# Kernel optimization log

Measured on AMD Instinct MI355X. Metric: run time of the kernel, lower is better.

Reference implementation:

```python
import jax, jax.numpy as jnp
from jax import lax
import numpy as np

B, T, S = 64, 1024, 1024  # batch, seq_len, hidden size


def setup_inputs() -> dict:
    key = jax.random.key(0)
    ks = jax.random.split(key, 7)
    bound = 1.0 / np.sqrt(S)  # PyTorch GRU/Linear default init: U(-1/sqrt(H), 1/sqrt(H))
    u = lambda k, shape: jax.random.uniform(k, shape, jnp.float32, -bound, bound)
    return {
        "batch": jax.random.normal(ks[0], (B, T, S), jnp.float32),
        "W_ih": u(ks[1], (3 * S, S)),   # [r; z; n] input weights
        "W_hh": u(ks[2], (3 * S, S)),   # [r; z; n] hidden weights
        "b_ih": u(ks[3], (3 * S,)),
        "b_hh": u(ks[4], (3 * S,)),
        "W_out": u(ks[5], (1, S)),
        "b_out": u(ks[6], (1,)),
    }


def reference(batch, W_ih, W_hh, b_ih, b_hh, W_out, b_out):
    # Precompute input projections for all timesteps with one big GEMM: [B,T,3S]
    x_gates = jnp.einsum("bts,gs->btg", batch, W_ih) + b_ih

    def step(h, xg):
        # h: [B,S], xg: [B,3S]
        hg = h @ W_hh.T + b_hh                      # [B,3S]
        xr, xz, xn = jnp.split(xg, 3, axis=-1)
        hr, hz, hn = jnp.split(hg, 3, axis=-1)
        r = jax.nn.sigmoid(xr + hr)
        z = jax.nn.sigmoid(xz + hz)
        n = jnp.tanh(xn + r * hn)
        h_new = (1.0 - z) * n + z * h               # PyTorch GRU update
        return h_new, None

    h0 = jnp.zeros((batch.shape[0], S), batch.dtype)
    hT, _ = lax.scan(step, h0, jnp.swapaxes(x_gates, 0, 1))  # scan over time

    # last-timestep hidden -> linear -> sigmoid -> squeeze
    out = jax.nn.sigmoid(hT @ W_out.T + b_out)  # [B,1]
    return out.squeeze(-1)                      # [B]
```

## Files before the change

kernel.cpp:

```cpp
#include <hip/hip_runtime.h>
#include <math.h>


#define BB 64
#define TT 1024
#define SS 1024
#define GG (3 * SS)
#define NBLK 256

__device__ unsigned g_sub[8 * 32];
__device__ unsigned g_cnt[32];
__device__ unsigned g_gen[32];

__global__ void init_bar_kernel() {
  for (int i = 0; i < 8 * 32; ++i) g_sub[i] = 0u;
  g_cnt[0] = 0u;
  g_gen[0] = 0u;
}

__global__ void zero_kernel(float* __restrict__ p) {
  p[(size_t)blockIdx.x * 1024 + threadIdx.x] = 0.f;
}

__global__ __launch_bounds__(256) void xgates_kernel(
    const float* __restrict__ A, const float* __restrict__ W,
    const float* __restrict__ b_ih, const float* __restrict__ b_hh,
    float* __restrict__ C) {
  __shared__ float As[16][132];
  __shared__ float Bs[16][132];

  const int tid = threadIdx.x;
  const int n0 = blockIdx.x * 128;
  const int t0 = blockIdx.y * 2;
  const int tx = tid & 15;
  const int ty = tid >> 4;

  float acc[8][8];
#pragma unroll
  for (int i = 0; i < 8; ++i)
#pragma unroll
    for (int j = 0; j < 8; ++j) acc[i][j] = 0.f;

  for (int kt = 0; kt < SS / 16; ++kt) {
    const int k0 = kt * 16;
#pragma unroll
    for (int i = 0; i < 2; ++i) {
      const int idx = tid + i * 256;
      const int r = idx >> 2;
      const int kq = (idx & 3) * 4;
      float4 av = *(const float4*)&A[((size_t)(r & 63) * TT + t0 + (r >> 6)) * SS + k0 + kq];
      float4 bv = *(const float4*)&W[(size_t)(n0 + r) * SS + k0 + kq];
      As[kq + 0][r] = av.x; As[kq + 1][r] = av.y;
      As[kq + 2][r] = av.z; As[kq + 3][r] = av.w;
      Bs[kq + 0][r] = bv.x; Bs[kq + 1][r] = bv.y;
      Bs[kq + 2][r] = bv.z; Bs[kq + 3][r] = bv.w;
    }
    __syncthreads();
#pragma unroll
    for (int k = 0; k < 16; ++k) {
      float4 a0 = *(const float4*)&As[k][ty * 8];
      float4 a1 = *(const float4*)&As[k][ty * 8 + 4];
      float4 b0 = *(const float4*)&Bs[k][tx * 8];
      float4 b1 = *(const float4*)&Bs[k][tx * 8 + 4];
      float a[8] = {a0.x, a0.y, a0.z, a0.w, a1.x, a1.y, a1.z, a1.w};
      float b[8] = {b0.x, b0.y, b0.z, b0.w, b1.x, b1.y, b1.z, b1.w};
#pragma unroll
      for (int i = 0; i < 8; ++i)
#pragma unroll
        for (int j = 0; j < 8; ++j) acc[i][j] = fmaf(a[i], b[j], acc[i][j]);
    }
    __syncthreads();
  }

  float bias[8];
#pragma unroll
  for (int j = 0; j < 8; ++j) {
    const int n = n0 + tx * 8 + j;
    bias[j] = b_ih[n] + (n < 2 * SS ? b_hh[n] : 0.f);
  }
  const int tt = t0 + (ty >> 3);
  const int bbase = (ty & 7) * 8;
#pragma unroll
  for (int j = 0; j < 8; ++j) {
    const int n = n0 + tx * 8 + j;
    const int g = n >> 10;
    const int u = n & 1023;
    const size_t o = ((size_t)(tt * 3 + g) * SS + u) * 64 + bbase;
    *(float4*)&C[o] = make_float4(acc[0][j] + bias[j], acc[1][j] + bias[j],
                                  acc[2][j] + bias[j], acc[3][j] + bias[j]);
    *(float4*)&C[o + 4] = make_float4(acc[4][j] + bias[j], acc[5][j] + bias[j],
                                      acc[6][j] + bias[j], acc[7][j] + bias[j]);
  }
}

__global__ __launch_bounds__(1024) void gru_persistent(
    const float* __restrict__ Whh, const float* __restrict__ xgT,
    const float* __restrict__ bhh, float* hA, float* hB) {
  __shared__ float part[16][64][13];
  __shared__ float sums[64][13];

  const int tid = threadIdx.x;
  const int lane = tid & 63;
  const int u0 = blockIdx.x * 4;
  const int wv = __builtin_amdgcn_readfirstlane(tid >> 6);
  const int k0 = wv * 64;
  const int ur = tid >> 6;

  const float* Wrow[12];
#pragma unroll
  for (int g = 0; g < 3; ++g)
#pragma unroll
    for (int r = 0; r < 4; ++r)
      Wrow[g * 4 + r] = Whh + (size_t)(g * SS + u0 + r) * SS + k0;

  float bhn = 0.f, xr = 0.f, xz = 0.f, xn = 0.f;
  if (tid < 256) {
    bhn = bhh[2 * SS + u0 + ur];
    const size_t xb = (size_t)(u0 + ur) * 64 + (size_t)lane;
    xr = xgT[xb];
    xz = xgT[xb + (size_t)SS * 64];
    xn = xgT[xb + (size_t)2 * SS * 64];
  }

  for (int t = 0; t < TT; ++t) {
    float* hin = (t & 1) ? hB : hA;
    float* hout = (t & 1) ? hA : hB;

    float hold = 0.f;
    if (tid < 256)
      hold = __hip_atomic_load(&hin[(u0 + ur) * 64 + lane], __ATOMIC_RELAXED,
                               __HIP_MEMORY_SCOPE_AGENT);

    float acc[12];
#pragma unroll
    for (int i = 0; i < 12; ++i) acc[i] = 0.f;

    for (int kk = 0; kk < 64; kk += 8) {
      float hv[8];
#pragma unroll
      for (int e = 0; e < 8; ++e)
        hv[e] = __hip_atomic_load(&hin[(size_t)(k0 + kk + e) * 64 + lane],
                                  __ATOMIC_RELAXED, __HIP_MEMORY_SCOPE_AGENT);
#pragma unroll
      for (int i = 0; i < 12; ++i) {
        const float* wp = Wrow[i] + kk;
        const float4 wa = *(const float4*)wp;
        const float4 wb = *(const float4*)(wp + 4);
        float a = acc[i];
        a = fmaf(hv[0], wa.x, a);
        a = fmaf(hv[1], wa.y, a);
        a = fmaf(hv[2], wa.z, a);
        a = fmaf(hv[3], wa.w, a);
        a = fmaf(hv[4], wb.x, a);
        a = fmaf(hv[5], wb.y, a);
        a = fmaf(hv[6], wb.z, a);
        a = fmaf(hv[7], wb.w, a);
        acc[i] = a;
      }
    }

    const int w = tid >> 6;
#pragma unroll
    for (int i = 0; i < 12; ++i) part[w][lane][i] = acc[i];
    __syncthreads();

    if (tid < 768) {
      const int sb = tid & 63, si = tid >> 6;
      float v = 0.f;
#pragma unroll
      for (int ww = 0; ww < 16; ++ww) v += part[ww][sb][si];
      sums[sb][si] = v;
    }
    __syncthreads();

    if (tid < 256) {
      const float ar = sums[lane][ur];
      const float az = sums[lane][4 + ur];
      const float an = sums[lane][8 + ur];
      const float rg = 1.f / (1.f + expf(-(xr + ar)));
      const float zg = 1.f / (1.f + expf(-(xz + az)));
      const float ng = tanhf(xn + rg * (an + bhn));
      const float hnew = (1.f - zg) * ng + zg * hold;
      __hip_atomic_store(&hout[(u0 + ur) * 64 + lane], hnew, __ATOMIC_RELAXED,
                         __HIP_MEMORY_SCOPE_AGENT);
      if (t + 1 < TT) {
        const size_t xb =
            ((size_t)((t + 1) * 3) * SS + u0 + ur) * 64 + (size_t)lane;
        xr = xgT[xb];
        xz = xgT[xb + (size_t)SS * 64];
        xn = xgT[xb + (size_t)2 * SS * 64];
      }
    }

    if (t != TT - 1) {
      __syncthreads();
      if (tid == 0) {
        bool done = false;
        const unsigned a = atomicAdd(&g_sub[(blockIdx.x & 7) * 32], 1u);
        if (a == 32u * (unsigned)(t + 1) - 1u) {
          const unsigned g = atomicAdd(&g_cnt[0], 1u);
          if (g == 8u * (unsigned)(t + 1) - 1u) {
            __hip_atomic_store(&g_gen[0], (unsigned)(t + 1), __ATOMIC_RELAXED,
                               __HIP_MEMORY_SCOPE_AGENT);
            done = true;
          }
        }
        if (!done) {
          while (__hip_atomic_load(&g_gen[0], __ATOMIC_RELAXED,
                                   __HIP_MEMORY_SCOPE_AGENT) <
                 (unsigned)(t + 1))
            __builtin_amdgcn_s_sleep(2);
        }
        __builtin_amdgcn_fence(__ATOMIC_ACQUIRE, "workgroup");
      }
      __syncthreads();
    }
  }
}

__global__ __launch_bounds__(256) void out_kernel(
    const float* __restrict__ hT, const float* __restrict__ Wout,
    const float* __restrict__ bout, float* __restrict__ out) {
  const int b = blockIdx.x;
  const int tid = threadIdx.x;
  float s = 0.f;
#pragma unroll
  for (int i = 0; i < 4; ++i) {
    const int u = tid + i * 256;
    s = fmaf(hT[(size_t)u * 64 + b], Wout[u], s);
  }
#pragma unroll
  for (int off = 32; off; off >>= 1) s += __shfl_down(s, off);
  __shared__ float red[4];
  if ((tid & 63) == 0) red[tid >> 6] = s;
  __syncthreads();
  if (tid == 0) {
    const float tot = red[0] + red[1] + red[2] + red[3] + bout[0];
    out[b] = 1.f / (1.f + expf(-tot));
  }
}

extern "C" void kernel_launch(void* const* d_in, const int* in_sizes, int n_in,
                              void* d_out, int out_size, void* d_ws,
                              size_t ws_size, hipStream_t stream) {
  const float* batch = (const float*)d_in[0];
  const float* W_ih = (const float*)d_in[1];
  const float* W_hh = (const float*)d_in[2];
  const float* b_ih = (const float*)d_in[3];
  const float* b_hh = (const float*)d_in[4];
  const float* W_out = (const float*)d_in[5];
  const float* b_out = (const float*)d_in[6];
  float* out = (float*)d_out;

  float* xgT = (float*)d_ws;
  float* hA = xgT + (size_t)TT * GG * BB;
  float* hB = hA + (size_t)SS * BB;

  init_bar_kernel<<<1, 1, 0, stream>>>();
  zero_kernel<<<BB, 1024, 0, stream>>>(hA);

  xgates_kernel<<<dim3(GG / 128, (BB * TT) / 128), 256, 0, stream>>>(
      batch, W_ih, b_ih, b_hh, xgT);

  {
    const float* a0 = W_hh;
    const float* a1 = xgT;
    const float* a2 = b_hh;
    float* a3 = hA;
    float* a4 = hB;
    void* args[5] = {&a0, &a1, &a2, &a3, &a4};
    hipLaunchCooperativeKernel((const void*)gru_persistent, dim3(NBLK),
                               dim3(1024), args, 0, stream);
  }

  out_kernel<<<BB, 256, 0, stream>>>(hA, W_out, b_out, out);
}
```

Before: 17.20 ms.

## Interleave hidden state layout for 64-bit loads, keep h in registers, prefetch x-gates

Changes the hidden-state buffer layout so each group of four units is stored interleaved per batch lane. Each wave can then fetch its h slice with batched 64-bit atomic loads issued up front, instead of scalar loads inside the k loop. The previous hidden value is kept in a register rather than reloaded, and the next step's x-gate loads are issued before the barrier so their latency overlaps the reduction. The change also adds a launch-bounds occupancy hint, shortens the spin sleep, and updates the output kernel to read the new layout. Holding 32 u64 values per thread raises register pressure.

```diff
diff --git a/kernel.cpp b/kernel.cpp
--- a/kernel.cpp
+++ b/kernel.cpp
@@ -7,6 +7,8 @@
 #define SS 1024
 #define GG (3 * SS)
 #define NBLK 256
+
+typedef unsigned long long u64;
 
 __device__ unsigned g_sub[8 * 32];
 __device__ unsigned g_cnt[32];
@@ -93,7 +95,7 @@
   }
 }
 
-__global__ __launch_bounds__(1024) void gru_persistent(
+__global__ __launch_bounds__(1024, 4) void gru_persistent(
     const float* __restrict__ Whh, const float* __restrict__ xgT,
     const float* __restrict__ bhh, float* hA, float* hB) {
   __shared__ float part[16][64][13];
@@ -113,7 +115,13 @@
     for (int r = 0; r < 4; ++r)
       Wrow[g * 4 + r] = Whh + (size_t)(g * SS + u0 + r) * SS + k0;
 
+  const u64* hA8 = (const u64*)hA + (size_t)(k0 >> 2) * 128 + lane * 2;
+  const u64* hB8 = (const u64*)hB + (size_t)(k0 >> 2) * 128 + lane * 2;
+  float* stA = hA + (size_t)u0 * 64 + lane * 4 + ur;
+  float* stB = hB + (size_t)u0 * 64 + lane * 4 + ur;
+
   float bhn = 0.f, xr = 0.f, xz = 0.f, xn = 0.f;
+  float hreg = 0.f;
   if (tid < 256) {
     bhn = bhh[2 * SS + u0 + ur];
     const size_t xb = (size_t)(u0 + ur) * 64 + (size_t)lane;
@@ -123,38 +131,42 @@
   }
 
   for (int t = 0; t < TT; ++t) {
-    float* hin = (t & 1) ? hB : hA;
-    float* hout = (t & 1) ? hA : hB;
-
-    float hold = 0.f;
-    if (tid < 256)
-      hold = __hip_atomic_load(&hin[(u0 + ur) * 64 + lane], __ATOMIC_RELAXED,
-                               __HIP_MEMORY_SCOPE_AGENT);
+    const u64* hp8 = (t & 1) ? hB8 : hA8;
+
+    u64 hv8[32];
+#pragma unroll
+    for (int q = 0; q < 16; ++q) {
+      hv8[2 * q] = __hip_atomic_load(hp8 + (size_t)q * 128, __ATOMIC_RELAXED,
+                                     __HIP_MEMORY_SCOPE_AGENT);
+      hv8[2 * q + 1] = __hip_atomic_load(hp8 + (size_t)q * 128 + 1,
+                                         __ATOMIC_RELAXED,
+                                         __HIP_MEMORY_SCOPE_AGENT);
+    }
 
     float acc[12];
 #pragma unroll
     for (int i = 0; i < 12; ++i) acc[i] = 0.f;
 
-    for (int kk = 0; kk < 64; kk += 8) {
-      float hv[8];
-#pragma unroll
-      for (int e = 0; e < 8; ++e)
-        hv[e] = __hip_atomic_load(&hin[(size_t)(k0 + kk + e) * 64 + lane],
-                                  __ATOMIC_RELAXED, __HIP_MEMORY_SCOPE_AGENT);
+#pragma unroll
+    for (int kk8 = 0; kk8 < 8; ++kk8) {
+      const float2 h0 = __builtin_bit_cast(float2, hv8[4 * kk8 + 0]);
+      const float2 h1 = __builtin_bit_cast(float2, hv8[4 * kk8 + 1]);
+      const float2 h2 = __builtin_bit_cast(float2, hv8[4 * kk8 + 2]);
+      const float2 h3 = __builtin_bit_cast(float2, hv8[4 * kk8 + 3]);
 #pragma unroll
       for (int i = 0; i < 12; ++i) {
-        const float* wp = Wrow[i] + kk;
+        const float* wp = Wrow[i] + kk8 * 8;
         const float4 wa = *(const float4*)wp;
         const float4 wb = *(const float4*)(wp + 4);
         float a = acc[i];
-        a = fmaf(hv[0], wa.x, a);
-        a = fmaf(hv[1], wa.y, a);
-        a = fmaf(hv[2], wa.z, a);
-        a = fmaf(hv[3], wa.w, a);
-        a = fmaf(hv[4], wb.x, a);
-        a = fmaf(hv[5], wb.y, a);
-        a = fmaf(hv[6], wb.z, a);
-        a = fmaf(hv[7], wb.w, a);
+        a = fmaf(h0.x, wa.x, a);
+        a = fmaf(h0.y, wa.y, a);
+        a = fmaf(h1.x, wa.z, a);
+        a = fmaf(h1.y, wa.w, a);
+        a = fmaf(h2.x, wb.x, a);
+        a = fmaf(h2.y, wb.y, a);
+        a = fmaf(h3.x, wb.z, a);
+        a = fmaf(h3.y, wb.w, a);
         acc[i] = a;
       }
     }
@@ -162,6 +174,15 @@
     const int w = tid >> 6;
 #pragma unroll
     for (int i = 0; i < 12; ++i) part[w][lane][i] = acc[i];
+
+    float nxr = 0.f, nxz = 0.f, nxn = 0.f;
+    if (tid < 256 && t + 1 < TT) {
+      const size_t xb =
+          ((size_t)((t + 1) * 3) * SS + u0 + ur) * 64 + (size_t)lane;
+      nxr = xgT[xb];
+      nxz = xgT[xb + (size_t)SS * 64];
+      nxn = xgT[xb + (size_t)2 * SS * 64];
+    }
     __syncthreads();
 
     if (tid < 768) {
@@ -180,16 +201,13 @@
       const float rg = 1.f / (1.f + expf(-(xr + ar)));
       const float zg = 1.f / (1.f + expf(-(xz + az)));
       const float ng = tanhf(xn + rg * (an + bhn));
-      const float hnew = (1.f - zg) * ng + zg * hold;
-      __hip_atomic_store(&hout[(u0 + ur) * 64 + lane], hnew, __ATOMIC_RELAXED,
-                         __HIP_MEMORY_SCOPE_AGENT);
-      if (t + 1 < TT) {
-        const size_t xb =
-            ((size_t)((t + 1) * 3) * SS + u0 + ur) * 64 + (size_t)lane;
-        xr = xgT[xb];
-        xz = xgT[xb + (size_t)SS * 64];
-        xn = xgT[xb + (size_t)2 * SS * 64];
-      }
+      const float hnew = (1.f - zg) * ng + zg * hreg;
+      hreg = hnew;
+      float* st = (t & 1) ? stA : stB;
+      __hip_atomic_store(st, hnew, __ATOMIC_RELAXED, __HIP_MEMORY_SCOPE_AGENT);
+      xr = nxr;
+      xz = nxz;
+      xn = nxn;
     }
 
     if (t != TT - 1) {
@@ -209,7 +227,7 @@
           while (__hip_atomic_load(&g_gen[0], __ATOMIC_RELAXED,
                                    __HIP_MEMORY_SCOPE_AGENT) <
                  (unsigned)(t + 1))
-            __builtin_amdgcn_s_sleep(2);
+            __builtin_amdgcn_s_sleep(1);
         }
         __builtin_amdgcn_fence(__ATOMIC_ACQUIRE, "workgroup");
       }
@@ -219,7 +237,7 @@
 }
 
 __global__ __launch_bounds__(256) void out_kernel(
-    const float* __restrict__ hT, const float* __restrict__ Wout,
+    const float* __restrict__ h4, const float* __restrict__ Wout,
     const float* __restrict__ bout, float* __restrict__ out) {
   const int b = blockIdx.x;
   const int tid = threadIdx.x;
@@ -227,7 +245,7 @@
 #pragma unroll
   for (int i = 0; i < 4; ++i) {
     const int u = tid + i * 256;
-    s = fmaf(hT[(size_t)u * 64 + b], Wout[u], s);
+    s = fmaf(h4[(size_t)(u >> 2) * 256 + b * 4 + (u & 3)], Wout[u], s);
   }
 #pragma unroll
   for (int off = 32; off; off >>= 1) s += __shfl_down(s, off);
```

Measured after the change: 21.01 ms. 1.22x slower.
